# Kernel tuning notes

Measured on AMD Instinct MI355X. Metric: run time of the kernel, lower is better.

Reference implementation:

```python
import jax, jax.numpy as jnp
import numpy as np

N, E, CIN, COUT = 50000, 800000, 61, 64
EPS = 1e-5


def batchnorm(h, g, b):
    # BatchNorm1d in training mode: batch stats (biased variance), affine
    m = jnp.mean(h, axis=0)
    v = jnp.var(h, axis=0)
    return g * (h - m) * jax.lax.rsqrt(v + EPS) + b


def setup_inputs() -> dict:
    key = jax.random.key(0)
    ks = jax.random.split(key, 7)
    x = jax.random.normal(ks[0], (N, CIN), jnp.float32)
    pos = jax.random.normal(ks[1], (N, 3), jnp.float32)
    edge_index = jax.random.randint(ks[2], (2, E), 0, N, dtype=jnp.int64)
    s1 = 1.0 / np.sqrt(CIN + 3)
    s2 = 1.0 / np.sqrt(COUT)
    ss = 1.0 / np.sqrt(CIN)
    W1 = jax.random.normal(ks[3], (CIN + 3, COUT), jnp.float32) * s1
    b1 = jnp.zeros((COUT,), jnp.float32)
    W2 = jax.random.normal(ks[4], (COUT, COUT), jnp.float32) * s2
    b2 = jnp.zeros((COUT,), jnp.float32)
    Ws = jax.random.normal(ks[5], (CIN, COUT), jnp.float32) * ss
    bs = jnp.zeros((COUT,), jnp.float32)
    ones = jnp.ones((COUT,), jnp.float32)
    zeros = jnp.zeros((COUT,), jnp.float32)
    return {
        "x": x, "pos": pos, "edge_index": edge_index,
        "W1": W1, "b1": b1, "g1": ones, "be1": zeros,
        "W2": W2, "b2": b2, "g2": ones, "be2": zeros,
        "Ws": Ws, "bs": bs, "gs": ones, "bes": zeros,
        "gf": ones, "bef": zeros,
    }


def reference(x, pos, edge_index, W1, b1, g1, be1, W2, b2, g2, be2,
              Ws, bs, gs, bes, gf, bef):
    src, dst = edge_index[0], edge_index[1]  # j -> i (source_to_target)
    # per-edge message: [x_j, pos_j - pos_i]  -> [E, CIN+3]
    msg = jnp.concatenate([x[src], pos[src] - pos[dst]], axis=-1)
    # local_nn = MLP([CIN+3, COUT, COUT]) with per-layer Lin -> ReLU -> BN
    h = batchnorm(jax.nn.relu(msg @ W1 + b1), g1, be1)
    h = batchnorm(jax.nn.relu(h @ W2 + b2), g2, be2)
    # scatter-max aggregation to destination nodes
    agg = jax.ops.segment_max(h, dst, num_segments=N)
    agg = jnp.where(jnp.isneginf(agg), 0.0, agg)  # nodes with no incoming edges
    # residual shortcut (Linear + BN since CIN != COUT)
    identity = batchnorm(x @ Ws + bs, gs, bes)
    return jax.nn.relu(batchnorm(agg, gf, bef) + identity)
```

## Files before the change

kernel.cpp:

```cpp
#include <hip/hip_runtime.h>

#define CIN 61
constexpr float EPS = 1e-5f;
constexpr double SCALE = 16777216.0;

using s16x8 = __attribute__((ext_vector_type(8))) short;
using fx4   = __attribute__((ext_vector_type(4))) float;

static __device__ __forceinline__ unsigned short f2bf(float f) {
  unsigned int u = __float_as_uint(f);
  u = (u + 0x7fffu + ((u >> 16) & 1u)) >> 16;
  return (unsigned short)u;
}
static __device__ __forceinline__ float bf2f(unsigned short h) {
  return __uint_as_float(((unsigned int)h) << 16);
}

__device__ __forceinline__ void stat_reduce(float val, float* red, long long* dst_ll) {
  int tid = threadIdx.x;
  red[tid] = val;
  __syncthreads();
  if (tid < 64) {
    float t = red[tid] + red[tid + 64] + red[tid + 128] + red[tid + 192];
    atomicAdd((unsigned long long*)&dst_ll[tid],
              (unsigned long long)(long long)((double)t * SCALE));
  }
  __syncthreads();
}

__global__ __launch_bounds__(256) void k_node(
    const float* __restrict__ x, const float* __restrict__ W1,
    const float* __restrict__ b1, const float* __restrict__ Ws,
    const float* __restrict__ bs, unsigned short* __restrict__ y,
    unsigned short* __restrict__ s_out, long long* __restrict__ stats, int N,
    const int* __restrict__ ei, unsigned int* __restrict__ hist,
    unsigned short* __restrict__ rank, int E) {
  const int tid = threadIdx.x, lane = tid & 63, wv = tid >> 6;
  float w1r[64], wsr[64];
#pragma unroll
  for (int k = 0; k < 64; ++k) {
    w1r[k] = (k < CIN) ? W1[k * 64 + lane] : 0.f;
    wsr[k] = (k < CIN) ? Ws[k * 64 + lane] : 0.f;
  }
  const float b1v = b1[lane], bsv = bs[lane];
  __shared__ float lrow[4][64];
  __shared__ float red[256];
  float ssum = 0.f, ssq = 0.f;
  const int nq = N >> 2;
  for (int q = blockIdx.x; q < nq; q += gridDim.x) {
    const int n = (q << 2) + wv;
    lrow[wv][lane] = (lane < CIN) ? x[(size_t)n * CIN + lane] : 0.f;
    __builtin_amdgcn_wave_barrier();
    float a0 = b1v, a1 = 0.f, a2 = 0.f, a3 = 0.f;
    float c0 = bsv, c1 = 0.f, c2 = 0.f, c3 = 0.f;
    const float4* rr = (const float4*)&lrow[wv][0];
#pragma unroll
    for (int k4 = 0; k4 < 16; ++k4) {
      float4 v = rr[k4];
      a0 = fmaf(v.x, w1r[4 * k4 + 0], a0);
      a1 = fmaf(v.y, w1r[4 * k4 + 1], a1);
      a2 = fmaf(v.z, w1r[4 * k4 + 2], a2);
      a3 = fmaf(v.w, w1r[4 * k4 + 3], a3);
      c0 = fmaf(v.x, wsr[4 * k4 + 0], c0);
      c1 = fmaf(v.y, wsr[4 * k4 + 1], c1);
      c2 = fmaf(v.z, wsr[4 * k4 + 2], c2);
      c3 = fmaf(v.w, wsr[4 * k4 + 3], c3);
    }
    y[(size_t)n * 64 + lane] = f2bf((a0 + a1) + (a2 + a3));
    const float sacc = (c0 + c1) + (c2 + c3);
    s_out[(size_t)n * 64 + lane] = f2bf(sacc);
    ssum += sacc;
    ssq = fmaf(sacc, sacc, ssq);
    __builtin_amdgcn_wave_barrier();
  }
  stat_reduce(ssum, red, stats + 256);
  stat_reduce(ssq, red, stats + 320);
  for (int i = blockIdx.x * 256 + tid; i < E; i += gridDim.x * 256) {
    const int dst = ei[E + i];
    rank[i] = (unsigned short)atomicAdd(&hist[dst], 1u);
  }
}

__global__ __launch_bounds__(256) void k_scan1(
    const unsigned int* __restrict__ hist, unsigned int* __restrict__ bsum) {
  const int tid = threadIdx.x, lane = tid & 63, wv = tid >> 6;
  const uint4 v = ((const uint4*)(hist + blockIdx.x * 1024))[tid];
  unsigned int s = v.x + v.y + v.z + v.w;
#pragma unroll
  for (int off = 1; off < 64; off <<= 1) s += __shfl_xor(s, off);
  __shared__ unsigned int wsum[4];
  if (lane == 0) wsum[wv] = s;
  __syncthreads();
  if (tid == 0) bsum[blockIdx.x] = wsum[0] + wsum[1] + wsum[2] + wsum[3];
}

__global__ void k_scan2(const unsigned int* __restrict__ bsum,
                        unsigned int* __restrict__ boff, int nb) {
  const int t = threadIdx.x;
  unsigned int v = (t < nb) ? bsum[t] : 0u;
  unsigned int incl = v;
#pragma unroll
  for (int off = 1; off < 64; off <<= 1) {
    unsigned int u = __shfl_up(incl, off);
    if (t >= off) incl += u;
  }
  if (t < nb) boff[t] = incl - v;
}

__global__ __launch_bounds__(256) void k_scan3(
    const unsigned int* __restrict__ hist, const unsigned int* __restrict__ boff,
    unsigned int* __restrict__ cursor0) {
  const int tid = threadIdx.x, lane = tid & 63, wv = tid >> 6;
  const uint4 v = ((const uint4*)(hist + blockIdx.x * 1024))[tid];
  const unsigned int s = v.x + v.y + v.z + v.w;
  unsigned int incl = s;
#pragma unroll
  for (int off = 1; off < 64; off <<= 1) {
    unsigned int u = __shfl_up(incl, off);
    if (lane >= off) incl += u;
  }
  __shared__ unsigned int wtot[4];
  if (lane == 63) wtot[wv] = incl;
  __syncthreads();
  unsigned int wb = boff[blockIdx.x];
#pragma unroll
  for (int k = 0; k < 4; ++k) wb += (k < wv) ? wtot[k] : 0u;
  const unsigned int ex = wb + incl - s;
  uint4 o;
  o.x = ex; o.y = ex + v.x; o.z = o.y + v.y; o.w = o.z + v.z;
  ((uint4*)(cursor0 + blockIdx.x * 1024))[tid] = o;
}

__global__ __launch_bounds__(256) void k_edge1(
    const int* __restrict__ ei, const float* __restrict__ pos,
    const unsigned short* __restrict__ y, const float* __restrict__ W1,
    const unsigned int* __restrict__ cursor0, const unsigned short* __restrict__ rank,
    int4* __restrict__ recS, long long* __restrict__ stats, int E) {
  const int tid = threadIdx.x, lane = tid & 63, wv = tid >> 6;
  const int g8 = lane >> 3, c8 = lane & 7;
  float wp[3][8];
#pragma unroll
  for (int d = 0; d < 3; ++d)
#pragma unroll
    for (int i = 0; i < 8; ++i) wp[d][i] = W1[(61 + d) * 64 + 8 * c8 + i];
  float ssum[8] = {0.f, 0.f, 0.f, 0.f, 0.f, 0.f, 0.f, 0.f};
  float ssq[8]  = {0.f, 0.f, 0.f, 0.f, 0.f, 0.f, 0.f, 0.f};
  const int ngrp = E >> 3;
  const int nw = gridDim.x * 4;
  for (int q = blockIdx.x * 4 + wv; q < ngrp; q += 4 * nw) {
    const int qB = q + nw, qC = q + 2 * nw, qD = q + 3 * nw;
    const bool hB = qB < ngrp, hC = qC < ngrp, hD = qD < ngrp;
    const int eA = (q << 3) + g8;
    const int eB = hB ? (qB << 3) + g8 : eA;
    const int eC = hC ? (qC << 3) + g8 : eA;
    const int eD = hD ? (qD << 3) + g8 : eA;
    const int srcA = ei[eA], dstA = ei[E + eA];
    const int srcB = ei[eB], dstB = ei[E + eB];
    const int srcC = ei[eC], dstC = ei[E + eC];
    const int srcD = ei[eD], dstD = ei[E + eD];
    float pvA = 0.f, pvB = 0.f, pvC = 0.f, pvD = 0.f;
    if (c8 < 3) {
      pvA = pos[srcA * 3 + c8] - pos[dstA * 3 + c8];
      pvB = pos[srcB * 3 + c8] - pos[dstB * 3 + c8];
      pvC = pos[srcC * 3 + c8] - pos[dstC * 3 + c8];
      pvD = pos[srcD * 3 + c8] - pos[dstD * 3 + c8];
    }
    const s16x8 yA = *(const s16x8*)(y + (unsigned)srcA * 64u + 8u * (unsigned)c8);
    const s16x8 yB = *(const s16x8*)(y + (unsigned)srcB * 64u + 8u * (unsigned)c8);
    const s16x8 yC = *(const s16x8*)(y + (unsigned)srcC * 64u + 8u * (unsigned)c8);
    const s16x8 yD = *(const s16x8*)(y + (unsigned)srcD * 64u + 8u * (unsigned)c8);
    unsigned offA = 0, offB = 0, offC = 0, offD = 0;
    if (c8 == 0) {
      offA = cursor0[dstA] + rank[eA];
      offB = cursor0[dstB] + rank[eB];
      offC = cursor0[dstC] + rank[eC];
      offD = cursor0[dstD] + rank[eD];
    }
#define EDGE1_BODY(SRC, DST, E_, PV, YV, OFF)                                   \
    {                                                                           \
      const float p0 = __shfl(PV, g8 * 8 + 0);                                  \
      const float p1 = __shfl(PV, g8 * 8 + 1);                                  \
      const float p2 = __shfl(PV, g8 * 8 + 2);                                  \
      _Pragma("unroll")                                                         \
      for (int i = 0; i < 8; ++i) {                                             \
        float v = bf2f((unsigned short)YV[i]);                                  \
        v = fmaf(p0, wp[0][i], v);                                              \
        v = fmaf(p1, wp[1][i], v);                                              \
        v = fmaf(p2, wp[2][i], v);                                              \
        v = fmaxf(v, 0.f);                                                      \
        ssum[i] += v;                                                           \
        ssq[i] = fmaf(v, v, ssq[i]);                                            \
      }                                                                         \
      if (c8 == 0) {                                                            \
        int4 r;                                                                 \
        r.x = (SRC & 0xffff) | (DST << 16);                                     \
        r.y = __float_as_int(p0);                                               \
        r.z = __float_as_int(p1);                                               \
        r.w = __float_as_int(p2);                                               \
        recS[OFF] = r;                                                          \
      }                                                                         \
    }
    EDGE1_BODY(srcA, dstA, eA, pvA, yA, offA)
    if (hB) EDGE1_BODY(srcB, dstB, eB, pvB, yB, offB)
    if (hC) EDGE1_BODY(srcC, dstC, eC, pvC, yC, offC)
    if (hD) EDGE1_BODY(srcD, dstD, eD, pvD, yD, offD)
#undef EDGE1_BODY
  }
#pragma unroll
  for (int i = 0; i < 8; ++i) {
    ssum[i] += __shfl_xor(ssum[i], 8);
    ssum[i] += __shfl_xor(ssum[i], 16);
    ssum[i] += __shfl_xor(ssum[i], 32);
    ssq[i] += __shfl_xor(ssq[i], 8);
    ssq[i] += __shfl_xor(ssq[i], 16);
    ssq[i] += __shfl_xor(ssq[i], 32);
  }
  __shared__ float sred[2][64];
  if (tid < 128) ((float*)sred)[tid] = 0.f;
  __syncthreads();
  if (g8 == 0) {
#pragma unroll
    for (int i = 0; i < 8; ++i) {
      atomicAdd(&sred[0][8 * c8 + i], ssum[i]);
      atomicAdd(&sred[1][8 * c8 + i], ssq[i]);
    }
  }
  __syncthreads();
  if (tid < 64) {
    atomicAdd((unsigned long long*)&stats[0 + tid],
              (unsigned long long)(long long)((double)sred[0][tid] * SCALE));
    atomicAdd((unsigned long long*)&stats[64 + tid],
              (unsigned long long)(long long)((double)sred[1][tid] * SCALE));
  }
}

__global__ void k_coefA(const long long* __restrict__ stats,
                        const float* __restrict__ g1, const float* __restrict__ be1,
                        const float* __restrict__ W2, const float* __restrict__ b2,
                        const float* __restrict__ W1,
                        unsigned short* __restrict__ bFpack,
                        float* __restrict__ wpPack, float* __restrict__ biasF,
                        double invE) {
  const int c = threadIdx.x;
  __shared__ float a1s[64], c1s[64], b2sh[64];
  double m = (double)stats[c] * invE;
  double v = (double)stats[64 + c] * invE - m * m;
  float a = g1[c] * rsqrtf((float)v + EPS);
  a1s[c] = a;
  c1s[c] = fmaf(-(float)m, a, be1[c]);
  __syncthreads();
  float acc = b2[c];
  for (int k = 0; k < 64; ++k) acc = fmaf(c1s[k], W2[k * 64 + c], acc);
  b2sh[c] = acc;
  const int lg = c >> 4, l15 = c & 15;
#pragma unroll
  for (int t = 0; t < 4; ++t)
#pragma unroll
    for (int s = 0; s < 2; ++s)
#pragma unroll
      for (int i = 0; i < 8; ++i) {
        const int k = s * 32 + lg * 8 + i;
        bFpack[c * 64 + t * 16 + s * 8 + i] = f2bf(a1s[k] * W2[k * 64 + l15 + 16 * t]);
      }
#pragma unroll
  for (int d = 0; d < 3; ++d)
#pragma unroll
    for (int j = 0; j < 16; ++j) {
      const int k = (j < 8) ? (lg * 8 + j) : (32 + lg * 8 + (j - 8));
      wpPack[c * 48 + d * 16 + j] = W1[(61 + d) * 64 + k];
    }
  __syncthreads();
  float4 bf;
  bf.x = b2sh[l15]; bf.y = b2sh[l15 + 16]; bf.z = b2sh[l15 + 32]; bf.w = b2sh[l15 + 48];
  ((float4*)biasF)[c] = bf;
}

__global__ __launch_bounds__(256) void k_edge2(
    const int4* __restrict__ recS, const unsigned short* __restrict__ y,
    const unsigned short* __restrict__ bFpack, const float* __restrict__ wpPack,
    const float* __restrict__ biasF, long long* __restrict__ stats,
    unsigned int* __restrict__ agg, int E) {
  const int tid = threadIdx.x, lane = tid & 63, wv = tid >> 6;
  const int l15 = lane & 15, lg = lane >> 4;
  s16x8 bF[4][2];
  {
    const s16x8* bfp = (const s16x8*)(bFpack + (size_t)lane * 64);
#pragma unroll
    for (int t = 0; t < 4; ++t)
#pragma unroll
      for (int s = 0; s < 2; ++s) bF[t][s] = bfp[t * 2 + s];
  }
  float wpA[3][8], wpB[3][8];
  {
    const float4* wpp = (const float4*)(wpPack + (size_t)lane * 48);
#pragma unroll
    for (int d = 0; d < 3; ++d) {
      const float4 q0 = wpp[d * 4 + 0], q1 = wpp[d * 4 + 1];
      const float4 q2 = wpp[d * 4 + 2], q3 = wpp[d * 4 + 3];
      wpA[d][0] = q0.x; wpA[d][1] = q0.y; wpA[d][2] = q0.z; wpA[d][3] = q0.w;
      wpA[d][4] = q1.x; wpA[d][5] = q1.y; wpA[d][6] = q1.z; wpA[d][7] = q1.w;
      wpB[d][0] = q2.x; wpB[d][1] = q2.y; wpB[d][2] = q2.z; wpB[d][3] = q2.w;
      wpB[d][4] = q3.x; wpB[d][5] = q3.y; wpB[d][6] = q3.z; wpB[d][7] = q3.w;
    }
  }
  float bias[4];
  {
    const float4 bv = ((const float4*)biasF)[lane];
    bias[0] = bv.x; bias[1] = bv.y; bias[2] = bv.z; bias[3] = bv.w;
  }
  __shared__ float ld2[4][16][68];
  float ssum[4] = {0.f, 0.f, 0.f, 0.f}, ssq[4] = {0.f, 0.f, 0.f, 0.f};
  const int nchunk = E >> 6;
  const int nw4 = gridDim.x * 4;
  for (int ch = blockIdx.x * 4 + wv; ch < nchunk; ch += nw4) {
    const int row0 = ch << 6;
    int4 rec = recS[row0 + l15];
    s16x8 yA, yB;
    {
      const unsigned srcP = (unsigned)rec.x & 0xffffu;
      const unsigned short* yr = y + srcP * 64u + (unsigned)(lg * 8);
      yA = *(const s16x8*)yr;
      yB = *(const s16x8*)(yr + 32);
    }
    int cur = -1;
    float m = 0.f;
    bool inside = false;
#pragma unroll
    for (int t4 = 0; t4 < 4; ++t4) {
      int4 recN;
      if (t4 < 3) recN = recS[row0 + ((t4 + 1) << 4) + l15];
      const int dstvCur = (int)(((unsigned)rec.x) >> 16);
      float p[3];
      p[0] = __int_as_float(rec.y);
      p[1] = __int_as_float(rec.z);
      p[2] = __int_as_float(rec.w);
      union { s16x8 v; unsigned int u[4]; } a0, a1;
#pragma unroll
      for (int h = 0; h < 4; ++h) {
        float f0 = bf2f((unsigned short)yA[2 * h]);
        float f1 = bf2f((unsigned short)yA[2 * h + 1]);
#pragma unroll
        for (int d = 0; d < 3; ++d) {
          f0 = fmaf(p[d], wpA[d][2 * h], f0);
          f1 = fmaf(p[d], wpA[d][2 * h + 1], f1);
        }
        f0 = fmaxf(f0, 0.f); f1 = fmaxf(f1, 0.f);
        asm("v_cvt_pk_bf16_f32 %0, %1, %2" : "=v"(a0.u[h]) : "v"(f0), "v"(f1));
        f0 = bf2f((unsigned short)yB[2 * h]);
        f1 = bf2f((unsigned short)yB[2 * h + 1]);
#pragma unroll
        for (int d = 0; d < 3; ++d) {
          f0 = fmaf(p[d], wpB[d][2 * h], f0);
          f1 = fmaf(p[d], wpB[d][2 * h + 1], f1);
        }
        f0 = fmaxf(f0, 0.f); f1 = fmaxf(f1, 0.f);
        asm("v_cvt_pk_bf16_f32 %0, %1, %2" : "=v"(a1.u[h]) : "v"(f0), "v"(f1));
      }
      fx4 acc[4];
#pragma unroll
      for (int t = 0; t < 4; ++t) {
        acc[t][0] = bias[t]; acc[t][1] = bias[t];
        acc[t][2] = bias[t]; acc[t][3] = bias[t];
      }
#pragma unroll
      for (int t = 0; t < 4; ++t) {
        acc[t] = __builtin_amdgcn_mfma_f32_16x16x32_bf16(a0.v, bF[t][0], acc[t], 0, 0, 0);
        acc[t] = __builtin_amdgcn_mfma_f32_16x16x32_bf16(a1.v, bF[t][1], acc[t], 0, 0, 0);
      }
#pragma unroll
      for (int t = 0; t < 4; ++t) {
        const int col = l15 + 16 * t;
#pragma unroll
        for (int j = 0; j < 4; ++j) {
          const float v = fmaxf(acc[t][j], 0.f);
          ssum[t] += v;
          ssq[t] = fmaf(v, v, ssq[t]);
          ld2[wv][lg * 4 + j][col] = v;
        }
      }
      __builtin_amdgcn_wave_barrier();
      s16x8 yAn, yBn;
      if (t4 < 3) {
        const unsigned srcN = (unsigned)recN.x & 0xffffu;
        const unsigned short* yrN = y + srcN * 64u + (unsigned)(lg * 8);
        yAn = *(const s16x8*)yrN;
        yBn = *(const s16x8*)(yrN + 32);
      }
      float v16[16];
#pragma unroll
      for (int r = 0; r < 16; ++r) v16[r] = ld2[wv][r][lane];
#pragma unroll
      for (int r = 0; r < 16; ++r) {
        const int d = __shfl(dstvCur, r);
        const float v = v16[r];
        if (d == cur) {
          m = fmaxf(m, v);
        } else {
          if (cur >= 0) {
            const unsigned int enc = __float_as_uint(m) | 0x80000000u;
            if (inside) agg[(unsigned)cur * 64u + lane] = enc;
            else atomicMax(&agg[(unsigned)cur * 64u + lane], enc);
          }
          cur = d;
          m = v;
          inside = (t4 > 0) || (r > 0);
        }
      }
      __builtin_amdgcn_wave_barrier();
      if (t4 < 3) { rec = recN; yA = yAn; yB = yBn; }
    }
    if (cur >= 0)
      atomicMax(&agg[(unsigned)cur * 64u + lane], __float_as_uint(m) | 0x80000000u);
  }
#pragma unroll
  for (int t = 0; t < 4; ++t) {
    ssum[t] += __shfl_xor(ssum[t], 16); ssum[t] += __shfl_xor(ssum[t], 32);
    ssq[t]  += __shfl_xor(ssq[t], 16);  ssq[t]  += __shfl_xor(ssq[t], 32);
  }
  __shared__ float sred[2][64];
  if (tid < 128) ((float*)sred)[tid] = 0.f;
  __syncthreads();
  if (lg == 0) {
#pragma unroll
    for (int t = 0; t < 4; ++t) {
      atomicAdd(&sred[0][l15 + 16 * t], ssum[t]);
      atomicAdd(&sred[1][l15 + 16 * t], ssq[t]);
    }
  }
  __syncthreads();
  if (tid < 64) {
    atomicAdd((unsigned long long*)&stats[128 + tid],
              (unsigned long long)(long long)((double)sred[0][tid] * SCALE));
    atomicAdd((unsigned long long*)&stats[192 + tid],
              (unsigned long long)(long long)((double)sred[1][tid] * SCALE));
  }
}

__global__ __launch_bounds__(256) void k_aggfix(
    const unsigned int* __restrict__ agg, long long* __restrict__ stats, int total) {
  const int tid = threadIdx.x;
  __shared__ float red[256];
  float ssum = 0.f, ssq = 0.f, kcf = 0.f;
  const int step = gridDim.x * 256;
  for (int i = blockIdx.x * 256 + tid; i < total; i += step) {
    const unsigned int u = agg[i];
    if (u >> 31) {
      const float v = __uint_as_float(u & 0x7fffffffu);
      ssum += v;
      ssq = fmaf(v, v, ssq);
      if ((i & 63) == 0) kcf += 1.f;
    }
  }
  stat_reduce(ssum, red, stats + 384);
  stat_reduce(ssq, red, stats + 448);
  stat_reduce(kcf, red, stats + 512);
}

__global__ void k_coefB(const long long* __restrict__ stats,
                        const float* __restrict__ g2, const float* __restrict__ be2,
                        const float* __restrict__ gs, const float* __restrict__ bes,
                        const float* __restrict__ gf, const float* __restrict__ bef,
                        float* __restrict__ coef, double invE, double invN, int N) {
  const int c = threadIdx.x;
  double m2 = (double)stats[128 + c] * invE;
  double v2 = (double)stats[192 + c] * invE - m2 * m2;
  float a2 = g2[c] * rsqrtf((float)v2 + EPS);
  float c2 = fmaf(-(float)m2, a2, be2[c]);
  double mS = (double)stats[256 + c] * invN;
  double vS = (double)stats[320 + c] * invN - mS * mS;
  float aS = gs[c] * rsqrtf((float)vS + EPS);
  float cS = fmaf(-(float)mS, aS, bes[c]);
  double su = (double)stats[384 + c] / SCALE;
  double qu = (double)stats[448 + c] / SCALE;
  double K  = (double)stats[512] / SCALE;
  double sv = (double)a2 * su + (double)c2 * K;
  double qv = (double)a2 * a2 * qu + 2.0 * a2 * c2 * su + (double)c2 * c2 * K;
  double mv = sv / N;
  double vv = qv / N - mv * mv;
  float aF = gf[c] * rsqrtf((float)vv + EPS);
  float cF = fmaf(-(float)mv, aF, bef[c]);
  coef[c]       = aF * a2;
  coef[64 + c]  = fmaf(aF, c2, cF);
  coef[128 + c] = cF;
  coef[192 + c] = aS;
  coef[256 + c] = cS;
}

__global__ __launch_bounds__(256) void k_final(
    const unsigned int* __restrict__ agg, const unsigned short* __restrict__ sbuf,
    const float* __restrict__ coef, float* __restrict__ out, int total) {
  int i = blockIdx.x * 256 + threadIdx.x;
  if (i >= total) return;
  const int c = i & 63;
  const unsigned int u = agg[i];
  float base;
  if (u >> 31)
    base = fmaf(coef[c], __uint_as_float(u & 0x7fffffffu), coef[64 + c]);
  else
    base = coef[128 + c];
  const float sv = fmaf(coef[192 + c], bf2f(sbuf[i]), coef[256 + c]);
  out[i] = fmaxf(base + sv, 0.f);
}

extern "C" void kernel_launch(void* const* d_in, const int* in_sizes, int n_in,
                              void* d_out, int out_size, void* d_ws, size_t ws_size,
                              hipStream_t stream) {
  const float* x   = (const float*)d_in[0];
  const float* pos = (const float*)d_in[1];
  const int*   ei  = (const int*)d_in[2];
  const float* W1  = (const float*)d_in[3];
  const float* b1  = (const float*)d_in[4];
  const float* g1  = (const float*)d_in[5];
  const float* be1 = (const float*)d_in[6];
  const float* W2  = (const float*)d_in[7];
  const float* b2  = (const float*)d_in[8];
  const float* g2  = (const float*)d_in[9];
  const float* be2 = (const float*)d_in[10];
  const float* Ws  = (const float*)d_in[11];
  const float* bs  = (const float*)d_in[12];
  const float* gs  = (const float*)d_in[13];
  const float* bes = (const float*)d_in[14];
  const float* gf  = (const float*)d_in[15];
  const float* bef = (const float*)d_in[16];
  const int N = in_sizes[0] / CIN;
  const int E = in_sizes[2] / 2;

  char* ws = (char*)d_ws;
  const size_t o_stats = 0;
  const size_t o_bsum  = 4608;
  const size_t o_boff  = 5120;
  const size_t o_hist  = 8192;
  const size_t o_agg   = o_hist + 200704;
  const size_t zeroEnd = o_agg + (size_t)N * 256;
  const size_t o_curs0 = zeroEnd;
  const size_t o_coef  = o_curs0 + 200704;
  const size_t o_frag  = o_coef + 4096;
  const size_t o_rank  = o_frag + 24576;
  const size_t o_rec   = o_rank + (size_t)E * 2;
  const size_t o_ybuf  = o_rec + (size_t)E * 16;
  const size_t o_sbuf  = o_ybuf + (size_t)N * 128;

  long long* stats      = (long long*)(ws + o_stats);
  unsigned int* bsum    = (unsigned int*)(ws + o_bsum);
  unsigned int* boff    = (unsigned int*)(ws + o_boff);
  unsigned int* hist    = (unsigned int*)(ws + o_hist);
  unsigned int* agg     = (unsigned int*)(ws + o_agg);
  unsigned int* cursor0 = (unsigned int*)(ws + o_curs0);
  float* coef           = (float*)(ws + o_coef);
  unsigned short* bFpack= (unsigned short*)(ws + o_frag);
  float* wpPack         = (float*)(ws + o_frag + 8192);
  float* biasF          = (float*)(ws + o_frag + 8192 + 12288);
  unsigned short* rank  = (unsigned short*)(ws + o_rank);
  int4* recS            = (int4*)(ws + o_rec);
  unsigned short* ybuf  = (unsigned short*)(ws + o_ybuf);
  unsigned short* sbuf  = (unsigned short*)(ws + o_sbuf);

  const double invE = 1.0 / (SCALE * (double)E);
  const double invN = 1.0 / (SCALE * (double)N);
  const int total = N * 64;
  const int nScanBlk = 49;

  hipMemsetAsync(d_ws, 0, zeroEnd, stream);

  hipLaunchKernelGGL(k_node, dim3(1024), dim3(256), 0, stream,
                     x, W1, b1, Ws, bs, ybuf, sbuf, stats, N, ei, hist, rank, E);
  hipLaunchKernelGGL(k_scan1, dim3(nScanBlk), dim3(256), 0, stream, hist, bsum);
  hipLaunchKernelGGL(k_scan2, dim3(1), dim3(64), 0, stream, bsum, boff, nScanBlk);
  hipLaunchKernelGGL(k_scan3, dim3(nScanBlk), dim3(256), 0, stream,
                     hist, boff, cursor0);
  hipLaunchKernelGGL(k_edge1, dim3(2048), dim3(256), 0, stream,
                     ei, pos, ybuf, W1, cursor0, rank, recS, stats, E);
  hipLaunchKernelGGL(k_coefA, dim3(1), dim3(64), 0, stream,
                     stats, g1, be1, W2, b2, W1, bFpack, wpPack, biasF, invE);
  hipLaunchKernelGGL(k_edge2, dim3(1563), dim3(256), 0, stream,
                     recS, ybuf, bFpack, wpPack, biasF, stats, agg, E);
  hipLaunchKernelGGL(k_aggfix, dim3(1024), dim3(256), 0, stream, agg, stats, total);
  hipLaunchKernelGGL(k_coefB, dim3(1), dim3(64), 0, stream,
                     stats, g2, be2, gs, bes, gf, bef, coef, invE, invN, N);
  hipLaunchKernelGGL(k_final, dim3((total + 255) / 256), dim3(256), 0, stream,
                     agg, sbuf, coef, (float*)d_out, total);
}
```

Baseline: 273.9 us.

## Materialize layer-1 bf16 activations in dst-sorted order instead of recomputing in edge2

The first edge kernel now writes each edge's full ReLU'd layer-1 activation row as bf16 into a dst-sorted buffer, and a new kernel fills a compact per-edge destination array. The second edge kernel then streams these rows directly into MFMA instead of gathering source features and recomputing the positional term. This removes random gathers and per-edge recompute but adds a large scattered write and sequential read of a 64-wide bf16 array per edge, plus extra workspace.

```diff
diff --git a/kernel.cpp b/kernel.cpp
--- a/kernel.cpp
+++ b/kernel.cpp
@@ -131,11 +131,21 @@
   ((uint4*)(cursor0 + blockIdx.x * 1024))[tid] = o;
 }
 
+__global__ __launch_bounds__(256) void k_dstfill(
+    const unsigned int* __restrict__ cursor0, unsigned short* __restrict__ dstS,
+    int N) {
+  const int d = blockIdx.x * 256 + threadIdx.x;
+  if (d >= N) return;
+  const unsigned int lo = cursor0[d];
+  const unsigned int hi = cursor0[d + 1];
+  for (unsigned int i = lo; i < hi; ++i) dstS[i] = (unsigned short)d;
+}
+
 __global__ __launch_bounds__(256) void k_edge1(
     const int* __restrict__ ei, const float* __restrict__ pos,
     const unsigned short* __restrict__ y, const float* __restrict__ W1,
     const unsigned int* __restrict__ cursor0, const unsigned short* __restrict__ rank,
-    int4* __restrict__ recS, long long* __restrict__ stats, int E) {
+    unsigned short* __restrict__ t1S, long long* __restrict__ stats, int E) {
   const int tid = threadIdx.x, lane = tid & 63, wv = tid >> 6;
   const int g8 = lane >> 3, c8 = lane & 7;
   float wp[3][8];
@@ -176,11 +186,13 @@
       offC = cursor0[dstC] + rank[eC];
       offD = cursor0[dstD] + rank[eD];
     }
-#define EDGE1_BODY(SRC, DST, E_, PV, YV, OFF)                                   \
+#define EDGE1_BODY(PV, YV, OFFV)                                                \
     {                                                                           \
       const float p0 = __shfl(PV, g8 * 8 + 0);                                  \
       const float p1 = __shfl(PV, g8 * 8 + 1);                                  \
       const float p2 = __shfl(PV, g8 * 8 + 2);                                  \
+      const unsigned off = __shfl(OFFV, g8 * 8 + 0);                            \
+      union { s16x8 v; unsigned short s[8]; } tb;                               \
       _Pragma("unroll")                                                         \
       for (int i = 0; i < 8; ++i) {                                             \
         float v = bf2f((unsigned short)YV[i]);                                  \
@@ -190,20 +202,14 @@
         v = fmaxf(v, 0.f);                                                      \
         ssum[i] += v;                                                           \
         ssq[i] = fmaf(v, v, ssq[i]);                                            \
+        tb.s[i] = f2bf(v);                                                      \
       }                                                                         \
-      if (c8 == 0) {                                                            \
-        int4 r;                                                                 \
-        r.x = (SRC & 0xffff) | (DST << 16);                                     \
-        r.y = __float_as_int(p0);                                               \
-        r.z = __float_as_int(p1);                                               \
-        r.w = __float_as_int(p2);                                               \
-        recS[OFF] = r;                                                          \
-      }                                                                         \
-    }
-    EDGE1_BODY(srcA, dstA, eA, pvA, yA, offA)
-    if (hB) EDGE1_BODY(srcB, dstB, eB, pvB, yB, offB)
-    if (hC) EDGE1_BODY(srcC, dstC, eC, pvC, yC, offC)
-    if (hD) EDGE1_BODY(srcD, dstD, eD, pvD, yD, offD)
+      *(s16x8*)(t1S + (size_t)off * 64 + 8 * c8) = tb.v;                        \
+    }
+    EDGE1_BODY(pvA, yA, offA)
+    if (hB) EDGE1_BODY(pvB, yB, offB)
+    if (hC) EDGE1_BODY(pvC, yC, offC)
+    if (hD) EDGE1_BODY(pvD, yD, offD)
 #undef EDGE1_BODY
   }
 #pragma unroll
@@ -237,10 +243,8 @@
 __global__ void k_coefA(const long long* __restrict__ stats,
                         const float* __restrict__ g1, const float* __restrict__ be1,
                         const float* __restrict__ W2, const float* __restrict__ b2,
-                        const float* __restrict__ W1,
                         unsigned short* __restrict__ bFpack,
-                        float* __restrict__ wpPack, float* __restrict__ biasF,
-                        double invE) {
+                        float* __restrict__ biasF, double invE) {
   const int c = threadIdx.x;
   __shared__ float a1s[64], c1s[64], b2sh[64];
   double m = (double)stats[c] * invE;
@@ -262,13 +266,6 @@
         const int k = s * 32 + lg * 8 + i;
         bFpack[c * 64 + t * 16 + s * 8 + i] = f2bf(a1s[k] * W2[k * 64 + l15 + 16 * t]);
       }
-#pragma unroll
-  for (int d = 0; d < 3; ++d)
-#pragma unroll
-    for (int j = 0; j < 16; ++j) {
-      const int k = (j < 8) ? (lg * 8 + j) : (32 + lg * 8 + (j - 8));
-      wpPack[c * 48 + d * 16 + j] = W1[(61 + d) * 64 + k];
-    }
   __syncthreads();
   float4 bf;
   bf.x = b2sh[l15]; bf.y = b2sh[l15 + 16]; bf.z = b2sh[l15 + 32]; bf.w = b2sh[l15 + 48];
@@ -276,10 +273,9 @@
 }
 
 __global__ __launch_bounds__(256) void k_edge2(
-    const int4* __restrict__ recS, const unsigned short* __restrict__ y,
-    const unsigned short* __restrict__ bFpack, const float* __restrict__ wpPack,
-    const float* __restrict__ biasF, long long* __restrict__ stats,
-    unsigned int* __restrict__ agg, int E) {
+    const unsigned short* __restrict__ t1S, const unsigned short* __restrict__ dstS,
+    const unsigned short* __restrict__ bFpack, const float* __restrict__ biasF,
+    long long* __restrict__ stats, unsigned int* __restrict__ agg, int E) {
   const int tid = threadIdx.x, lane = tid & 63, wv = tid >> 6;
   const int l15 = lane & 15, lg = lane >> 4;
   s16x8 bF[4][2];
@@ -289,19 +285,6 @@
     for (int t = 0; t < 4; ++t)
 #pragma unroll
       for (int s = 0; s < 2; ++s) bF[t][s] = bfp[t * 2 + s];
-  }
-  float wpA[3][8], wpB[3][8];
-  {
-    const float4* wpp = (const float4*)(wpPack + (size_t)lane * 48);
-#pragma unroll
-    for (int d = 0; d < 3; ++d) {
-      const float4 q0 = wpp[d * 4 + 0], q1 = wpp[d * 4 + 1];
-      const float4 q2 = wpp[d * 4 + 2], q3 = wpp[d * 4 + 3];
-      wpA[d][0] = q0.x; wpA[d][1] = q0.y; wpA[d][2] = q0.z; wpA[d][3] = q0.w;
-      wpA[d][4] = q1.x; wpA[d][5] = q1.y; wpA[d][6] = q1.z; wpA[d][7] = q1.w;
-      wpB[d][0] = q2.x; wpB[d][1] = q2.y; wpB[d][2] = q2.z; wpB[d][3] = q2.w;
-      wpB[d][4] = q3.x; wpB[d][5] = q3.y; wpB[d][6] = q3.z; wpB[d][7] = q3.w;
-    }
   }
   float bias[4];
   {
@@ -314,48 +297,16 @@
   const int nw4 = gridDim.x * 4;
   for (int ch = blockIdx.x * 4 + wv; ch < nchunk; ch += nw4) {
     const int row0 = ch << 6;
-    int4 rec = recS[row0 + l15];
-    s16x8 yA, yB;
-    {
-      const unsigned srcP = (unsigned)rec.x & 0xffffu;
-      const unsigned short* yr = y + srcP * 64u + (unsigned)(lg * 8);
-      yA = *(const s16x8*)yr;
-      yB = *(const s16x8*)(yr + 32);
-    }
     int cur = -1;
     float m = 0.f;
     bool inside = false;
 #pragma unroll
     for (int t4 = 0; t4 < 4; ++t4) {
-      int4 recN;
-      if (t4 < 3) recN = recS[row0 + ((t4 + 1) << 4) + l15];
-      const int dstvCur = (int)(((unsigned)rec.x) >> 16);
-      float p[3];
-      p[0] = __int_as_float(rec.y);
-      p[1] = __int_as_float(rec.z);
-      p[2] = __int_as_float(rec.w);
-      union { s16x8 v; unsigned int u[4]; } a0, a1;
-#pragma unroll
-      for (int h = 0; h < 4; ++h) {
-        float f0 = bf2f((unsigned short)yA[2 * h]);
-        float f1 = bf2f((unsigned short)yA[2 * h + 1]);
-#pragma unroll
-        for (int d = 0; d < 3; ++d) {
-          f0 = fmaf(p[d], wpA[d][2 * h], f0);
-          f1 = fmaf(p[d], wpA[d][2 * h + 1], f1);
-        }
-        f0 = fmaxf(f0, 0.f); f1 = fmaxf(f1, 0.f);
-        asm("v_cvt_pk_bf16_f32 %0, %1, %2" : "=v"(a0.u[h]) : "v"(f0), "v"(f1));
-        f0 = bf2f((unsigned short)yB[2 * h]);
-        f1 = bf2f((unsigned short)yB[2 * h + 1]);
-#pragma unroll
-        for (int d = 0; d < 3; ++d) {
-          f0 = fmaf(p[d], wpB[d][2 * h], f0);
-          f1 = fmaf(p[d], wpB[d][2 * h + 1], f1);
-        }
-        f0 = fmaxf(f0, 0.f); f1 = fmaxf(f1, 0.f);
-        asm("v_cvt_pk_bf16_f32 %0, %1, %2" : "=v"(a1.u[h]) : "v"(f0), "v"(f1));
-      }
+      const int rbase = row0 + (t4 << 4);
+      const unsigned short* ar = t1S + (size_t)(rbase + l15) * 64 + (unsigned)(lg * 8);
+      const s16x8 aF0 = *(const s16x8*)ar;
+      const s16x8 aF1 = *(const s16x8*)(ar + 32);
+      const int dstv = (int)dstS[rbase + l15];
       fx4 acc[4];
 #pragma unroll
       for (int t = 0; t < 4; ++t) {
@@ -364,8 +315,8 @@
       }
 #pragma unroll
       for (int t = 0; t < 4; ++t) {
-        acc[t] = __builtin_amdgcn_mfma_f32_16x16x32_bf16(a0.v, bF[t][0], acc[t], 0, 0, 0);
-        acc[t] = __builtin_amdgcn_mfma_f32_16x16x32_bf16(a1.v, bF[t][1], acc[t], 0, 0, 0);
+        acc[t] = __builtin_amdgcn_mfma_f32_16x16x32_bf16(aF0, bF[t][0], acc[t], 0, 0, 0);
+        acc[t] = __builtin_amdgcn_mfma_f32_16x16x32_bf16(aF1, bF[t][1], acc[t], 0, 0, 0);
       }
 #pragma unroll
       for (int t = 0; t < 4; ++t) {
@@ -379,19 +330,12 @@
         }
       }
       __builtin_amdgcn_wave_barrier();
-      s16x8 yAn, yBn;
-      if (t4 < 3) {
-        const unsigned srcN = (unsigned)recN.x & 0xffffu;
-        const unsigned short* yrN = y + srcN * 64u + (unsigned)(lg * 8);
-        yAn = *(const s16x8*)yrN;
-        yBn = *(const s16x8*)(yrN + 32);
-      }
       float v16[16];
 #pragma unroll
       for (int r = 0; r < 16; ++r) v16[r] = ld2[wv][r][lane];
 #pragma unroll
       for (int r = 0; r < 16; ++r) {
-        const int d = __shfl(dstvCur, r);
+        const int d = __shfl(dstv, r);
         const float v = v16[r];
         if (d == cur) {
           m = fmaxf(m, v);
@@ -407,7 +351,6 @@
         }
       }
       __builtin_amdgcn_wave_barrier();
-      if (t4 < 3) { rec = recN; yA = yAn; yB = yBn; }
     }
     if (cur >= 0)
       atomicMax(&agg[(unsigned)cur * 64u + lane], __float_as_uint(m) | 0x80000000u);
@@ -535,10 +478,11 @@
   const size_t o_curs0 = zeroEnd;
   const size_t o_coef  = o_curs0 + 200704;
   const size_t o_frag  = o_coef + 4096;
-  const size_t o_rank  = o_frag + 24576;
-  const size_t o_rec   = o_rank + (size_t)E * 2;
-  const size_t o_ybuf  = o_rec + (size_t)E * 16;
+  const size_t o_rank  = o_frag + 12288;
+  const size_t o_dstS  = o_rank + (size_t)E * 2;
+  const size_t o_ybuf  = o_dstS + (size_t)E * 2;
   const size_t o_sbuf  = o_ybuf + (size_t)N * 128;
+  const size_t o_t1S   = o_sbuf + (size_t)N * 128;
 
   long long* stats      = (long long*)(ws + o_stats);
   unsigned int* bsum    = (unsigned int*)(ws + o_bsum);
@@ -548,12 +492,12 @@
   unsigned int* cursor0 = (unsigned int*)(ws + o_curs0);
   float* coef           = (float*)(ws + o_coef);
   unsigned short* bFpack= (unsigned short*)(ws + o_frag);
-  float* wpPack         = (float*)(ws + o_frag + 8192);
-  float* biasF          = (float*)(ws + o_frag + 8192 + 12288);
+  float* biasF          = (float*)(ws + o_frag + 8192);
   unsigned short* rank  = (unsigned short*)(ws + o_rank);
-  int4* recS            = (int4*)(ws + o_rec);
+  unsigned short* dstS  = (unsigned short*)(ws + o_dstS);
   unsigned short* ybuf  = (unsigned short*)(ws + o_ybuf);
   unsigned short* sbuf  = (unsigned short*)(ws + o_sbuf);
+  unsigned short* t1S   = (unsigned short*)(ws + o_t1S);
 
   const double invE = 1.0 / (SCALE * (double)E);
   const double invN = 1.0 / (SCALE * (double)N);
@@ -568,12 +512,14 @@
   hipLaunchKernelGGL(k_scan2, dim3(1), dim3(64), 0, stream, bsum, boff, nScanBlk);
   hipLaunchKernelGGL(k_scan3, dim3(nScanBlk), dim3(256), 0, stream,
                      hist, boff, cursor0);
+  hipLaunchKernelGGL(k_dstfill, dim3((N + 255) / 256), dim3(256), 0, stream,
+                     cursor0, dstS, N);
   hipLaunchKernelGGL(k_edge1, dim3(2048), dim3(256), 0, stream,
-                     ei, pos, ybuf, W1, cursor0, rank, recS, stats, E);
+                     ei, pos, ybuf, W1, cursor0, rank, t1S, stats, E);
   hipLaunchKernelGGL(k_coefA, dim3(1), dim3(64), 0, stream,
-                     stats, g1, be1, W2, b2, W1, bFpack, wpPack, biasF, invE);
+                     stats, g1, be1, W2, b2, bFpack, biasF, invE);
   hipLaunchKernelGGL(k_edge2, dim3(1563), dim3(256), 0, stream,
-                     recS, ybuf, bFpack, wpPack, biasF, stats, agg, E);
+                     t1S, dstS, bFpack, biasF, stats, agg, E);
   hipLaunchKernelGGL(k_aggfix, dim3(1024), dim3(256), 0, stream, agg, stats, total);
   hipLaunchKernelGGL(k_coefB, dim3(1), dim3(64), 0, stream,
                      stats, g2, be2, gs, bes, gf, bef, coef, invE, invN, N);
```

New measurement: 277.6 us. No clear change (+1.3%).
